# Optimization experiments

Hardware: AMD Instinct MI355X
Metric: run time of the kernel (lower is better)

Reference implementation:

```python
import jax, jax.numpy as jnp
import numpy as np

N_NODES, N_EDGES, IN_DIM, HID, N_FEAT_CLOSE, N_GRAPHS = 100000, 1600000, 128, 64, 5, 512


def _glorot(k, shape):
    lim = float(np.sqrt(6.0 / (shape[0] + shape[1])))
    return jax.random.uniform(k, shape, jnp.float32, -lim, lim)


def setup_inputs() -> dict:
    key = jax.random.key(0)
    ks = jax.random.split(key, 16)
    x = jax.random.normal(ks[0], (N_NODES, IN_DIM), jnp.float32)
    edge_index = jax.random.randint(ks[1], (2, N_EDGES), 0, N_NODES, jnp.int32)
    closeness = jax.random.uniform(ks[2], (N_NODES, N_FEAT_CLOSE), jnp.float32)
    batch = jnp.sort(jax.random.randint(ks[3], (N_NODES,), 0, N_GRAPHS, jnp.int32))
    return {
        'x': x, 'edge_index': edge_index, 'closeness': closeness, 'batch': batch,
        'num_graphs': N_GRAPHS,
        'W1': _glorot(ks[4], (IN_DIM, HID)), 'b1': jnp.zeros((HID,), jnp.float32),
        'W2': _glorot(ks[5], (HID, HID)), 'b2': jnp.zeros((HID,), jnp.float32),
        'W3': _glorot(ks[6], (HID, HID)), 'b3': jnp.zeros((HID,), jnp.float32),
        'Wc': _glorot(ks[7], (N_FEAT_CLOSE, 1)), 'bc': jnp.zeros((1,), jnp.float32),
        'Wa1': _glorot(ks[8], (HID, 16)), 'ba1': jnp.zeros((16,), jnp.float32),
        'Wa2': _glorot(ks[9], (16, 1)), 'ba2': jnp.zeros((1,), jnp.float32),
    }


def reference(x, edge_index, closeness, batch, num_graphs, W1, b1, W2, b2, W3, b3, Wc, bc, Wa1, ba1, Wa2, ba2):
    src, dst = edge_index[0], edge_index[1]
    N = x.shape[0]
    # GCN symmetric normalization with implicit self-loops (weight 1)
    deg = jax.ops.segment_sum(jnp.ones(src.shape, x.dtype), dst, num_segments=N) + 1.0
    dinv = jax.lax.rsqrt(deg)
    norm = dinv[src] * dinv[dst]  # [E]
    self_norm = (dinv * dinv)[:, None]  # 1/deg, self-loop coefficient

    def gcn(h, W, b):
        h = h @ W  # [N, hid]
        agg = jax.ops.segment_sum(h[src] * norm[:, None], dst, num_segments=N)
        return jax.nn.relu(agg + h * self_norm + b)

    h = gcn(x, W1, b1)
    h = gcn(h, W2, b2)
    h = gcn(h, W3, b3)

    # per-graph softmax over closeness scores, scaled by graph size
    s = closeness @ Wc + bc  # [N,1]
    smax = jax.ops.segment_max(s, batch, num_segments=num_graphs)
    e = jnp.exp(s - smax[batch])
    ssum = jax.ops.segment_sum(e, batch, num_segments=num_graphs)
    counts = jax.ops.segment_sum(jnp.ones((N,), x.dtype), batch, num_segments=num_graphs)
    w = (e / ssum[batch]) * counts[batch][:, None]  # [N,1]

    # weighted per-graph max pooling, then tiny MLP per graph
    pooled = jax.ops.segment_max(w * h, batch, num_segments=num_graphs)  # [G,64]
    a = jax.nn.relu(pooled @ Wa1 + ba1)
    return a @ Wa2 + ba2  # [G,1]
```

## Files before the change

### kernel.cpp

```cpp
#include <hip/hip_runtime.h>

#define N_NODESC 100000
#define N_EDGESC 1600000
#define IN_DIMC 128
#define HIDC 64
#define N_GRAPHSC 512
#define PAD_DEG 64


__global__ void zero_bounds_kernel(int* __restrict__ cntR, const int* __restrict__ batch,
                                   int* __restrict__ gstart) {
  int i = blockIdx.x * blockDim.x + threadIdx.x;
  if (i >= N_NODESC) return;
  cntR[i] = 0;
  cntR[N_NODESC + i] = 0;
  cntR[2 * N_NODESC + i] = 0;
  cntR[3 * N_NODESC + i] = 0;
  int b = batch[i];
  int prev = (i == 0) ? -1 : batch[i - 1];
  for (int g = prev + 1; g <= b; ++g) gstart[g] = i;
  if (i == N_NODESC - 1)
    for (int g = b + 1; g <= N_GRAPHSC; ++g) gstart[g] = N_NODESC;
}

__global__ void deg_kernel(const int* __restrict__ dstv, int* __restrict__ cntR,
                           int* __restrict__ slot) {
  int e4 = (blockIdx.x * blockDim.x + threadIdx.x) * 4;
  if (e4 >= N_EDGESC) return;
  int4 d = *(const int4*)(dstv + e4);
  int4 s;
  s.x = atomicAdd(&cntR[d.x], 1);
  s.y = atomicAdd(&cntR[N_NODESC + d.y], 1);
  s.z = atomicAdd(&cntR[2 * N_NODESC + d.z], 1);
  s.w = atomicAdd(&cntR[3 * N_NODESC + d.w], 1);
  *(int4*)(slot + e4) = s;
}

__global__ void off_dinv_kernel(const int* __restrict__ cntR, int* __restrict__ offR,
                                int* __restrict__ cnt, float* __restrict__ dinv) {
  int i = blockIdx.x * blockDim.x + threadIdx.x;
  if (i >= N_NODESC) return;
  int c0 = cntR[i];
  int c1 = cntR[N_NODESC + i];
  int c2 = cntR[2 * N_NODESC + i];
  int c3 = cntR[3 * N_NODESC + i];
  offR[i] = c0;
  offR[N_NODESC + i] = c0 + c1;
  offR[2 * N_NODESC + i] = c0 + c1 + c2;
  int tot = c0 + c1 + c2 + c3;
  cnt[i] = tot;
  dinv[i] = rsqrtf((float)tot + 1.0f);
}

__global__ void fill_pad_kernel(const int* __restrict__ srcv, const int* __restrict__ dstv,
                                const int* __restrict__ slot, const int* __restrict__ offR,
                                int* __restrict__ csr_pad) {
  int e4 = (blockIdx.x * blockDim.x + threadIdx.x) * 4;
  if (e4 >= N_EDGESC) return;
  int4 s = *(const int4*)(srcv + e4);
  int4 d = *(const int4*)(dstv + e4);
  int4 sl = *(const int4*)(slot + e4);
  int p0 = sl.x;
  int p1 = offR[d.y] + sl.y;
  int p2 = offR[N_NODESC + d.z] + sl.z;
  int p3 = offR[2 * N_NODESC + d.w] + sl.w;
  if (p0 < PAD_DEG) __builtin_nontemporal_store(s.x, &csr_pad[d.x * PAD_DEG + p0]);
  if (p1 < PAD_DEG) __builtin_nontemporal_store(s.y, &csr_pad[d.y * PAD_DEG + p1]);
  if (p2 < PAD_DEG) __builtin_nontemporal_store(s.z, &csr_pad[d.z * PAD_DEG + p2]);
  if (p3 < PAD_DEG) __builtin_nontemporal_store(s.w, &csr_pad[d.w * PAD_DEG + p3]);
}

#define GR_M 256
#define GR_KC 16
#define XS_STRIDE 288
#define GR_BLOCKS ((N_NODESC + GR_M - 1) / GR_M)

__device__ __forceinline__ int pcol(int r) { return r + 4 * (r >> 5); }

template <int KT>
__global__ void __launch_bounds__(128, 2)
gemm_rc_kernel(const float* __restrict__ X, const float* __restrict__ W,
               const float* __restrict__ dinv, float* __restrict__ T) {
  __shared__ float xs[GR_KC * XS_STRIDE];
  __shared__ float ws[GR_KC * 64];
  int t = threadIdx.x;
  int base = blockIdx.x * GR_M;
  int rg = t >> 2;
  int cg = t & 3;
  int r0 = rg * 8;
  int c0 = cg * 16;
  int kq = cg * 4;
  int px = pcol(r0);

  float4 acc[8][4];
#pragma unroll
  for (int i = 0; i < 8; ++i)
#pragma unroll
    for (int j = 0; j < 4; ++j) acc[i][j] = make_float4(0.f, 0.f, 0.f, 0.f);

  for (int kb = 0; kb < KT; kb += GR_KC) {
    if (kb) __syncthreads();
    float4 xv[8];
#pragma unroll
    for (int i = 0; i < 8; ++i) {
      int row = base + r0 + i;
      if (row >= N_NODESC) row = N_NODESC - 1;
      xv[i] = *(const float4*)(X + (size_t)row * KT + kb + kq);
    }
#pragma unroll
    for (int c = 0; c < 4; ++c) {
      const float* a = (const float*)xv;
      float4 w0 = make_float4(a[0 * 4 + c], a[1 * 4 + c], a[2 * 4 + c], a[3 * 4 + c]);
      float4 w1 = make_float4(a[4 * 4 + c], a[5 * 4 + c], a[6 * 4 + c], a[7 * 4 + c]);
      *(float4*)(xs + (kq + c) * XS_STRIDE + px) = w0;
      *(float4*)(xs + (kq + c) * XS_STRIDE + px + 4) = w1;
    }
#pragma unroll
    for (int j = 0; j < 2; ++j) {
      int f = t * 2 + j;
      int kl = f >> 4;
      int c4 = (f & 15) * 4;
      *(float4*)(ws + kl * 64 + c4) = *(const float4*)(W + (size_t)(kb + kl) * HIDC + c4);
    }
    __syncthreads();
#pragma unroll
    for (int k = 0; k < GR_KC; ++k) {
      float4 xa = *(const float4*)(xs + k * XS_STRIDE + px);
      float4 xb = *(const float4*)(xs + k * XS_STRIDE + px + 4);
      float4 wv[4];
#pragma unroll
      for (int j = 0; j < 4; ++j) wv[j] = *(const float4*)(ws + k * 64 + c0 + 4 * j);
      float xf[8] = {xa.x, xa.y, xa.z, xa.w, xb.x, xb.y, xb.z, xb.w};
#pragma unroll
      for (int i = 0; i < 8; ++i)
#pragma unroll
        for (int j = 0; j < 4; ++j) {
          acc[i][j].x = fmaf(xf[i], wv[j].x, acc[i][j].x);
          acc[i][j].y = fmaf(xf[i], wv[j].y, acc[i][j].y);
          acc[i][j].z = fmaf(xf[i], wv[j].z, acc[i][j].z);
          acc[i][j].w = fmaf(xf[i], wv[j].w, acc[i][j].w);
        }
    }
  }
#pragma unroll
  for (int i = 0; i < 8; ++i) {
    int row = base + r0 + i;
    if (row < N_NODESC) {
      float dv = dinv[row];
#pragma unroll
      for (int j = 0; j < 4; ++j) {
        float4 o;
        o.x = acc[i][j].x * dv;
        o.y = acc[i][j].y * dv;
        o.z = acc[i][j].z * dv;
        o.w = acc[i][j].w * dv;
        *(float4*)(T + (size_t)row * HIDC + c0 + 4 * j) = o;
      }
    }
  }
}

__global__ void gather_kernel(const float* __restrict__ ts, const float* __restrict__ dinv,
                              const int* __restrict__ cnt, const int* __restrict__ csr_pad,
                              const float* __restrict__ bias, float* __restrict__ h) {
  int lane = threadIdx.x & 63;
  int node = (blockIdx.x * blockDim.x + threadIdx.x) >> 6;
  if (node >= N_NODESC) return;
  int q = lane >> 4;
  int c = lane & 15;
  int deg = min(cnt[node], PAD_DEG);
  const int* __restrict__ row = csr_pad + node * PAD_DEG;
  const float4* __restrict__ ts4 = (const float4*)ts;
  float4 acc = make_float4(0.f, 0.f, 0.f, 0.f);
  int e = 0;
  for (; e + 16 <= deg; e += 16) {
    int s0 = row[e + q];
    int s1 = row[e + 4 + q];
    int s2 = row[e + 8 + q];
    int s3 = row[e + 12 + q];
    float4 v0 = ts4[s0 * 16 + c];
    float4 v1 = ts4[s1 * 16 + c];
    float4 v2 = ts4[s2 * 16 + c];
    float4 v3 = ts4[s3 * 16 + c];
    acc.x += (v0.x + v1.x) + (v2.x + v3.x);
    acc.y += (v0.y + v1.y) + (v2.y + v3.y);
    acc.z += (v0.z + v1.z) + (v2.z + v3.z);
    acc.w += (v0.w + v1.w) + (v2.w + v3.w);
  }
  for (; e + 4 <= deg; e += 4) {
    int s0 = row[e + q];
    float4 v = ts4[s0 * 16 + c];
    acc.x += v.x;
    acc.y += v.y;
    acc.z += v.z;
    acc.w += v.w;
  }
  if (e < deg && q < deg - e) {
    int s0 = row[e + q];
    float4 v = ts4[s0 * 16 + c];
    acc.x += v.x;
    acc.y += v.y;
    acc.z += v.z;
    acc.w += v.w;
  }
  acc.x += __shfl_xor(acc.x, 16);
  acc.y += __shfl_xor(acc.y, 16);
  acc.z += __shfl_xor(acc.z, 16);
  acc.w += __shfl_xor(acc.w, 16);
  acc.x += __shfl_xor(acc.x, 32);
  acc.y += __shfl_xor(acc.y, 32);
  acc.z += __shfl_xor(acc.z, 32);
  acc.w += __shfl_xor(acc.w, 32);
  if (q == 0) {
    float4 self = ts4[node * 16 + c];
    float4 bv = ((const float4*)bias)[c];
    float dv = dinv[node];
    float4 o;
    o.x = fmaxf(fmaf(acc.x + self.x, dv, bv.x), 0.f);
    o.y = fmaxf(fmaf(acc.y + self.y, dv, bv.y), 0.f);
    o.z = fmaxf(fmaf(acc.z + self.z, dv, bv.z), 0.f);
    o.w = fmaxf(fmaf(acc.w + self.w, dv, bv.w), 0.f);
    ((float4*)h)[node * 16 + c] = o;
  }
}

__global__ void __launch_bounds__(256)
readout_kernel(const float* __restrict__ h, const float* __restrict__ closeness,
               const float* __restrict__ Wc, const float* __restrict__ bc,
               const int* __restrict__ gstart, const float* __restrict__ Wa1,
               const float* __restrict__ ba1, const float* __restrict__ Wa2,
               const float* __restrict__ ba2, float* __restrict__ out) {
  __shared__ float sArr[1024];
  __shared__ float red[256];
  __shared__ float cross[4 * 64];
  int g = blockIdx.x;
  int t = threadIdx.x;
  int n0 = gstart[g], n1 = gstart[g + 1];
  int count = n1 - n0;
  int cap = min(count, 1024);
  float wc0 = Wc[0], wc1 = Wc[1], wc2 = Wc[2], wc3 = Wc[3], wc4 = Wc[4], bcv = bc[0];
  float lmax = -3.4e38f;
  for (int idx = t; idx < cap; idx += 256) {
    const float* c = closeness + (size_t)(n0 + idx) * 5;
    float s = fmaf(c[4], wc4, fmaf(c[3], wc3, fmaf(c[2], wc2, fmaf(c[1], wc1, fmaf(c[0], wc0, bcv)))));
    sArr[idx] = s;
    lmax = fmaxf(lmax, s);
  }
  red[t] = lmax;
  __syncthreads();
  for (int s = 128; s > 0; s >>= 1) {
    if (t < s) red[t] = fmaxf(red[t], red[t + s]);
    __syncthreads();
  }
  float m = red[0];
  __syncthreads();
  float lsum = 0.f;
  for (int idx = t; idx < cap; idx += 256) {
    float e = expf(sArr[idx] - m);
    sArr[idx] = e;
    lsum += e;
  }
  red[t] = lsum;
  __syncthreads();
  for (int s = 128; s > 0; s >>= 1) {
    if (t < s) red[t] += red[t + s];
    __syncthreads();
  }
  float scale = (count > 0) ? ((float)count / red[0]) : 0.f;
  __syncthreads();
  int wv = t >> 6, lane = t & 63;
  float pmax = 0.f;
  for (int idx = wv; idx < cap; idx += 4) {
    float w = sArr[idx] * scale;
    pmax = fmaxf(pmax, w * h[(size_t)(n0 + idx) * HIDC + lane]);
  }
  cross[wv * 64 + lane] = pmax;
  __syncthreads();
  if (wv == 0) {
    float p = fmaxf(fmaxf(cross[lane], cross[64 + lane]),
                    fmaxf(cross[128 + lane], cross[192 + lane]));
    float o = 0.f;
#pragma unroll
    for (int tt = 0; tt < 16; ++tt) {
      float prod = p * Wa1[lane * 16 + tt];
#pragma unroll
      for (int off = 32; off > 0; off >>= 1) prod += __shfl_xor(prod, off);
      float a = fmaxf(prod + ba1[tt], 0.f);
      o += a * Wa2[tt];
    }
    if (lane == 0) out[g] = o + ba2[0];
  }
}


extern "C" void kernel_launch(void* const* d_in, const int* in_sizes, int n_in,
                              void* d_out, int out_size, void* d_ws, size_t ws_size,
                              hipStream_t stream) {
  const float* x = (const float*)d_in[0];
  const int* ei = (const int*)d_in[1];
  const float* closeness = (const float*)d_in[2];
  const int* batch = (const int*)d_in[3];
  const float* W1 = (const float*)d_in[5];
  const float* b1 = (const float*)d_in[6];
  const float* W2 = (const float*)d_in[7];
  const float* b2 = (const float*)d_in[8];
  const float* W3 = (const float*)d_in[9];
  const float* b3 = (const float*)d_in[10];
  const float* Wc = (const float*)d_in[11];
  const float* bc = (const float*)d_in[12];
  const float* Wa1 = (const float*)d_in[13];
  const float* ba1 = (const float*)d_in[14];
  const float* Wa2 = (const float*)d_in[15];
  const float* ba2 = (const float*)d_in[16];
  float* out = (float*)d_out;
  const int* srcv = ei;
  const int* dstv = ei + N_EDGESC;

  char* ws = (char*)d_ws;
  size_t off = 0;
  auto alloc = [&](size_t bytes) -> void* {
    void* p = ws + off;
    off = (off + bytes + 255) & ~(size_t)255;
    return p;
  };
  float* tbuf = (float*)alloc(sizeof(float) * N_NODESC * HIDC);
  float* hbuf = (float*)alloc(sizeof(float) * N_NODESC * HIDC);
  int* csr_pad = (int*)alloc(sizeof(int) * N_NODESC * PAD_DEG);
  int* slot = (int*)alloc(sizeof(int) * N_EDGESC);
  int* cntR = (int*)alloc(sizeof(int) * N_NODESC * 4);
  int* offR = (int*)alloc(sizeof(int) * N_NODESC * 3);
  int* cnt = (int*)alloc(sizeof(int) * N_NODESC);
  float* dinv = (float*)alloc(sizeof(float) * N_NODESC);
  int* gstart = (int*)alloc(sizeof(int) * (N_GRAPHSC + 1));

  const int B = 256;
  int gN = (N_NODESC + B - 1) / B;
  int gE4 = (N_EDGESC / 4 + B - 1) / B;
  int gGather = (N_NODESC * 64) / B;

  zero_bounds_kernel<<<gN, B, 0, stream>>>(cntR, batch, gstart);
  deg_kernel<<<gE4, B, 0, stream>>>(dstv, cntR, slot);
  off_dinv_kernel<<<gN, B, 0, stream>>>(cntR, offR, cnt, dinv);
  fill_pad_kernel<<<gE4, B, 0, stream>>>(srcv, dstv, slot, offR, csr_pad);

  gemm_rc_kernel<IN_DIMC><<<GR_BLOCKS, 128, 0, stream>>>(x, W1, dinv, tbuf);
  gather_kernel<<<gGather, B, 0, stream>>>(tbuf, dinv, cnt, csr_pad, b1, hbuf);
  gemm_rc_kernel<HIDC><<<GR_BLOCKS, 128, 0, stream>>>(hbuf, W2, dinv, tbuf);
  gather_kernel<<<gGather, B, 0, stream>>>(tbuf, dinv, cnt, csr_pad, b2, hbuf);
  gemm_rc_kernel<HIDC><<<GR_BLOCKS, 128, 0, stream>>>(hbuf, W3, dinv, tbuf);
  gather_kernel<<<gGather, B, 0, stream>>>(tbuf, dinv, cnt, csr_pad, b3, hbuf);

  readout_kernel<<<N_GRAPHSC, B, 0, stream>>>(hbuf, closeness, Wc, bc, gstart,
                                              Wa1, ba1, Wa2, ba2, out);
}
```

Measured before the change: 555.0 us.

## Replace block GEMM with single-wave double-buffered GEMM without barriers

Replaces the 128-thread, 256-row GEMM with a 64-thread (one-wavefront) kernel covering 128 rows per block. It double-buffers the X and W tiles in LDS and prefetches the next K-chunk into registers while computing the current one. Because the block is a single wavefront, all __syncthreads barriers are removed, and each lane now loads its own W row directly. The aims are to overlap global loads with FMA work and to drop barrier stalls. The risks are relying on in-order LDS behaviour within a wave instead of explicit barriers, and lower per-CU occupancy flexibility from the tiny blocks.

```diff
diff --git a/kernel.cpp b/kernel.cpp
--- a/kernel.cpp
+++ b/kernel.cpp
@@ -70,27 +70,25 @@
   if (p3 < PAD_DEG) __builtin_nontemporal_store(s.w, &csr_pad[d.w * PAD_DEG + p3]);
 }
 
-#define GR_M 256
-#define GR_KC 16
-#define XS_STRIDE 288
-#define GR_BLOCKS ((N_NODESC + GR_M - 1) / GR_M)
-
-__device__ __forceinline__ int pcol(int r) { return r + 4 * (r >> 5); }
+#define GW_KC 16
+#define GW_ST 144
+#define GW_WST 68
+#define GW_BLOCKS ((N_NODESC + 127) / 128)
 
 template <int KT>
-__global__ void __launch_bounds__(128, 2)
-gemm_rc_kernel(const float* __restrict__ X, const float* __restrict__ W,
-               const float* __restrict__ dinv, float* __restrict__ T) {
-  __shared__ float xs[GR_KC * XS_STRIDE];
-  __shared__ float ws[GR_KC * 64];
-  int t = threadIdx.x;
-  int base = blockIdx.x * GR_M;
-  int rg = t >> 2;
-  int cg = t & 3;
+__global__ void __launch_bounds__(64)
+gemm_wave_kernel(const float* __restrict__ X, const float* __restrict__ W,
+                 const float* __restrict__ dinv, float* __restrict__ T) {
+  __shared__ float xs[2][GW_KC * GW_ST];
+  __shared__ float ws[2][GW_KC * GW_WST];
+  int l = threadIdx.x;
+  int rg = l >> 2;
+  int cg = l & 3;
   int r0 = rg * 8;
   int c0 = cg * 16;
   int kq = cg * 4;
-  int px = pcol(r0);
+  int px = r0 + 4 * (r0 >> 5);
+  int base = blockIdx.x * 128;
 
   float4 acc[8][4];
 #pragma unroll
@@ -98,9 +96,10 @@
 #pragma unroll
     for (int j = 0; j < 4; ++j) acc[i][j] = make_float4(0.f, 0.f, 0.f, 0.f);
 
-  for (int kb = 0; kb < KT; kb += GR_KC) {
-    if (kb) __syncthreads();
-    float4 xv[8];
+  float4 xv[8];
+  float4 wv[4];
+
+  auto gload = [&](int kb) {
 #pragma unroll
     for (int i = 0; i < 8; ++i) {
       int row = base + r0 + i;
@@ -108,40 +107,51 @@
       xv[i] = *(const float4*)(X + (size_t)row * KT + kb + kq);
     }
 #pragma unroll
+    for (int j = 0; j < 4; ++j)
+      wv[j] = *(const float4*)(W + (size_t)(kb + rg) * HIDC + c0 + 4 * j);
+  };
+
+  auto sstore = [&](int b) {
+    const float* a = (const float*)xv;
+#pragma unroll
     for (int c = 0; c < 4; ++c) {
-      const float* a = (const float*)xv;
-      float4 w0 = make_float4(a[0 * 4 + c], a[1 * 4 + c], a[2 * 4 + c], a[3 * 4 + c]);
-      float4 w1 = make_float4(a[4 * 4 + c], a[5 * 4 + c], a[6 * 4 + c], a[7 * 4 + c]);
-      *(float4*)(xs + (kq + c) * XS_STRIDE + px) = w0;
-      *(float4*)(xs + (kq + c) * XS_STRIDE + px + 4) = w1;
-    }
-#pragma unroll
-    for (int j = 0; j < 2; ++j) {
-      int f = t * 2 + j;
-      int kl = f >> 4;
-      int c4 = (f & 15) * 4;
-      *(float4*)(ws + kl * 64 + c4) = *(const float4*)(W + (size_t)(kb + kl) * HIDC + c4);
-    }
-    __syncthreads();
-#pragma unroll
-    for (int k = 0; k < GR_KC; ++k) {
-      float4 xa = *(const float4*)(xs + k * XS_STRIDE + px);
-      float4 xb = *(const float4*)(xs + k * XS_STRIDE + px + 4);
-      float4 wv[4];
-#pragma unroll
-      for (int j = 0; j < 4; ++j) wv[j] = *(const float4*)(ws + k * 64 + c0 + 4 * j);
+      float4 lo = make_float4(a[0 * 4 + c], a[1 * 4 + c], a[2 * 4 + c], a[3 * 4 + c]);
+      float4 hi = make_float4(a[4 * 4 + c], a[5 * 4 + c], a[6 * 4 + c], a[7 * 4 + c]);
+      *(float4*)(&xs[b][(kq + c) * GW_ST + px]) = lo;
+      *(float4*)(&xs[b][(kq + c) * GW_ST + px + 4]) = hi;
+    }
+#pragma unroll
+    for (int j = 0; j < 4; ++j)
+      *(float4*)(&ws[b][rg * GW_WST + c0 + 4 * j]) = wv[j];
+  };
+
+  gload(0);
+  sstore(0);
+  constexpr int NB = KT / GW_KC;
+  for (int t = 0; t < NB; ++t) {
+    int b = t & 1;
+    if (t + 1 < NB) gload((t + 1) * GW_KC);
+#pragma unroll
+    for (int k = 0; k < GW_KC; ++k) {
+      float4 xa = *(const float4*)(&xs[b][k * GW_ST + px]);
+      float4 xb = *(const float4*)(&xs[b][k * GW_ST + px + 4]);
+      float4 wq[4];
+#pragma unroll
+      for (int j = 0; j < 4; ++j) wq[j] = *(const float4*)(&ws[b][k * GW_WST + c0 + 4 * j]);
       float xf[8] = {xa.x, xa.y, xa.z, xa.w, xb.x, xb.y, xb.z, xb.w};
 #pragma unroll
       for (int i = 0; i < 8; ++i)
 #pragma unroll
         for (int j = 0; j < 4; ++j) {
-          acc[i][j].x = fmaf(xf[i], wv[j].x, acc[i][j].x);
-          acc[i][j].y = fmaf(xf[i], wv[j].y, acc[i][j].y);
-          acc[i][j].z = fmaf(xf[i], wv[j].z, acc[i][j].z);
-          acc[i][j].w = fmaf(xf[i], wv[j].w, acc[i][j].w);
+          acc[i][j].x = fmaf(xf[i], wq[j].x, acc[i][j].x);
+          acc[i][j].y = fmaf(xf[i], wq[j].y, acc[i][j].y);
+          acc[i][j].z = fmaf(xf[i], wq[j].z, acc[i][j].z);
+          acc[i][j].w = fmaf(xf[i], wq[j].w, acc[i][j].w);
         }
     }
-  }
+    if (t + 1 < NB) sstore((t + 1) & 1);
+  }
+
 #pragma unroll
   for (int i = 0; i < 8; ++i) {
     int row = base + r0 + i;
@@ -343,11 +353,11 @@
   off_dinv_kernel<<<gN, B, 0, stream>>>(cntR, offR, cnt, dinv);
   fill_pad_kernel<<<gE4, B, 0, stream>>>(srcv, dstv, slot, offR, csr_pad);
 
-  gemm_rc_kernel<IN_DIMC><<<GR_BLOCKS, 128, 0, stream>>>(x, W1, dinv, tbuf);
+  gemm_wave_kernel<IN_DIMC><<<GW_BLOCKS, 64, 0, stream>>>(x, W1, dinv, tbuf);
   gather_kernel<<<gGather, B, 0, stream>>>(tbuf, dinv, cnt, csr_pad, b1, hbuf);
-  gemm_rc_kernel<HIDC><<<GR_BLOCKS, 128, 0, stream>>>(hbuf, W2, dinv, tbuf);
+  gemm_wave_kernel<HIDC><<<GW_BLOCKS, 64, 0, stream>>>(hbuf, W2, dinv, tbuf);
   gather_kernel<<<gGather, B, 0, stream>>>(tbuf, dinv, cnt, csr_pad, b2, hbuf);
-  gemm_rc_kernel<HIDC><<<GR_BLOCKS, 128, 0, stream>>>(hbuf, W3, dinv, tbuf);
+  gemm_wave_kernel<HIDC><<<GW_BLOCKS, 64, 0, stream>>>(hbuf, W3, dinv, tbuf);
   gather_kernel<<<gGather, B, 0, stream>>>(tbuf, dinv, cnt, csr_pad, b3, hbuf);
 
   readout_kernel<<<N_GRAPHSC, B, 0, stream>>>(hbuf, closeness, Wc, bc, gstart,
```

New measurement: 657.8 us. +18.5%, slower.
